# Kernel optimization log

Hardware: AMD Instinct MI355X
Metric: run time of the kernel (lower is better)

## Reference

```python
import jax, jax.numpy as jnp
import numpy as np

GENRES = 20; TAGS = 1000; GTAGS = 1128; MOVIES = 20000; YEARS = 120; TBINS = 128
B = 1024; HIST = 50; PH = 256; OD = 128
EG = 8; ET = 16; EGT = 16; EM = 32; EY = 8; EUG = 32; ETS = 4
PAD = MOVIES  # padding index; context buffers have MOVIES+1 rows, last row = zeros


def setup_inputs():
    ks = iter(jax.random.split(jax.random.key(0), 64))
    nrm = lambda shp, s=0.1: (s * jax.random.normal(next(ks), shp)).astype(jnp.float32)
    P = MOVIES + 1
    genome_ctx = jax.random.uniform(next(ks), (P, GTAGS), dtype=jnp.float32).at[-1].set(0.0)
    genre_ctx = jax.random.uniform(next(ks), (P, GENRES), dtype=jnp.float32).at[-1].set(0.0)
    tag_ctx = jax.random.uniform(next(ks), (P, TAGS), dtype=jnp.float32).at[-1].set(0.0)
    year_ctx = jax.random.randint(next(ks), (P,), 0, YEARS).at[-1].set(0)
    return dict(
        user_genre_contexts=jax.random.uniform(next(ks), (B, GENRES), dtype=jnp.float32),
        user_watch_history=jax.random.randint(next(ks), (B, HIST), 0, P),
        user_watch_history_ratings=5.0 * jax.random.uniform(next(ks), (B, HIST), dtype=jnp.float32),
        timestamps=jax.random.randint(next(ks), (B,), 0, TBINS),
        target_movieId=jax.random.randint(next(ks), (B,), 0, MOVIES),
        genome_ctx=genome_ctx, genre_ctx=genre_ctx, tag_ctx=tag_ctx, year_ctx=year_ctx,
        item_emb=nrm((P, EM), 0.01).at[-1].set(0.0),  # padding_idx row zeroed
        year_emb_tab=nrm((YEARS, EY), 0.01),
        ts_emb_tab=nrm((TBINS, ETS), 0.01),
        w_item=nrm((EM, EM)), b_item=jnp.zeros((EM,), jnp.float32),
        w_genre=nrm((GENRES, EG)), b_genre=jnp.zeros((EG,), jnp.float32),
        w_tag=nrm((TAGS, ET)), b_tag=jnp.zeros((ET,), jnp.float32),
        w_genome=nrm((GTAGS, EGT)), b_genome=jnp.zeros((EGT,), jnp.float32),
        w_year=nrm((EY, EY)), b_year=jnp.zeros((EY,), jnp.float32),
        w_ugenre=nrm((GENRES, EUG)), b_ugenre=jnp.zeros((EUG,), jnp.float32),
        w_ts=nrm((ETS, ETS)), b_ts=jnp.zeros((ETS,), jnp.float32),
        w_up1=nrm((OD + EGT + EUG + ETS, PH)), b_up1=jnp.zeros((PH,), jnp.float32),
        w_up2=nrm((PH, OD)), b_up2=jnp.zeros((OD,), jnp.float32),
        w_ip1=nrm((EG + ET + EGT + EM + EY, PH)), b_ip1=jnp.zeros((PH,), jnp.float32),
        w_ip2=nrm((PH, OD)), b_ip2=jnp.zeros((OD,), jnp.float32),
    )


def reference(user_genre_contexts, user_watch_history, user_watch_history_ratings,
              timestamps, target_movieId, genome_ctx, genre_ctx, tag_ctx, year_ctx,
              item_emb, year_emb_tab, ts_emb_tab,
              w_item, b_item, w_genre, b_genre, w_tag, b_tag, w_genome, b_genome,
              w_year, b_year, w_ugenre, b_ugenre, w_ts, b_ts,
              w_up1, b_up1, w_up2, b_up2, w_ip1, b_ip1, w_ip2, b_ip2):
    lt = lambda x, W, b: jnp.tanh(x @ W + b)

    def item_tower(mg, mt, mgt, yr, ids):
        # concat of five small Linear+Tanh towers, then 2-layer projection MLP
        cat = jnp.concatenate([
            lt(mg, w_genre, b_genre), lt(mt, w_tag, b_tag), lt(mgt, w_genome, b_genome),
            lt(item_emb[ids], w_item, b_item), lt(year_emb_tab[yr], w_year, b_year)], axis=-1)
        return jax.nn.relu(cat @ w_ip1 + b_ip1) @ w_ip2 + b_ip2

    Bn, Hn = user_watch_history.shape
    pad_mask = (user_watch_history != PAD).astype(jnp.float32)[..., None]       # (B,H,1)
    rating_weights = user_watch_history_ratings[..., None] * pad_mask            # (B,H,1)
    weight_sum = jnp.clip(jnp.abs(rating_weights).sum(axis=1), 1e-6)             # (B,1)

    # item pool: full item-tower embeddings of watched movies, rating-weighted avg
    flat = user_watch_history.reshape(-1)
    embs = item_tower(genre_ctx[flat], tag_ctx[flat], genome_ctx[flat],
                      year_ctx[flat], flat).reshape(Bn, Hn, OD)
    item_pool = (embs * rating_weights).sum(axis=1) / weight_sum                 # (B,OD)

    # genome pool (kept separately in use_item_pool_for_history mode)
    genome_embs = lt(genome_ctx[user_watch_history], w_genome, b_genome)         # (B,H,EGT)
    genome_emb = (genome_embs * rating_weights).sum(axis=1) / weight_sum

    genre_emb = lt(user_genre_contexts, w_ugenre, b_ugenre)
    ts_emb = lt(ts_emb_tab[timestamps], w_ts, b_ts)
    user_cat = jnp.concatenate([item_pool, genome_emb, genre_emb, ts_emb], axis=1)
    user = jax.nn.relu(user_cat @ w_up1 + b_up1) @ w_up2 + b_up2                 # (B,OD)

    item = item_tower(genre_ctx[target_movieId], tag_ctx[target_movieId],
                      genome_ctx[target_movieId], year_ctx[target_movieId], target_movieId)
    return jnp.einsum('bd,bd->b', user, item)
```

## Files before the change

### kernel.cpp

```cpp
#include <hip/hip_runtime.h>
#include <hip/hip_bf16.h>

typedef __bf16 bf16x8 __attribute__((ext_vector_type(8)));
typedef __bf16 bf16x4 __attribute__((ext_vector_type(4)));
typedef float  f32x4  __attribute__((ext_vector_type(4)));

namespace {
constexpr int P       = 20001;
constexpr int NT_TILE = 1251;
constexpr int PROWS   = NT_TILE * 16;
constexpr int NGENRES = 20;
constexpr int NTAGS   = 1000;
constexpr int NGTAGS  = 1128;
constexpr int NB      = 1024;
constexpr int NH      = 50;
constexpr int PHID    = 256;
constexpr int OD      = 128;
constexpr int EG = 8, ET = 16, EGT = 16, EM = 32, EY = 8, EUG = 32, ETS = 4;
constexpr int PAD  = 20000;
constexpr int SAW  = 1160;
constexpr int SC   = 104;
constexpr int SH   = 264;
constexpr int UC   = 192;
constexpr int UCS  = 200;
constexpr int KC_TAG = 32, KC_GEN = 36;
constexpr int KC_IP1 = 3,  NT_IP1 = 16;
constexpr int KC_IP2 = 8,  NT_IP2 = 8;
constexpr int KC_UP1 = 6,  NT_UP1 = 16;
constexpr int KC_UP2 = 8,  NT_UP2 = 8;
}

static __device__ __forceinline__ f32x4 mfma16(bf16x8 a, bf16x8 b, f32x4 c) {
  return __builtin_amdgcn_mfma_f32_16x16x32_bf16(a, b, c, 0, 0, 0);
}

__global__ __launch_bounds__(512) void setup_wf_kernel(
    const float* __restrict__ w_tag, const float* __restrict__ w_genome,
    const float* __restrict__ w_ip1, const float* __restrict__ w_ip2,
    const float* __restrict__ w_up1, const float* __restrict__ w_up2,
    __bf16* __restrict__ Wtf, __bf16* __restrict__ Wgf,
    __bf16* __restrict__ Wip1f, __bf16* __restrict__ Wip2f,
    __bf16* __restrict__ Wup1f, __bf16* __restrict__ Wup2f)
{
  const int b = blockIdx.x, t = threadIdx.x;
  const int l = t >> 3, j = t & 7;
  const int krow = (l >> 4) * 8 + j, l15 = l & 15;
  const float* src; __bf16* dst; int K, N, kc, nt;
  if (b < 32)        { src = w_tag;    dst = Wtf   + (long)b * 512;       K = NTAGS;  N = 16;  kc = b;      nt = 0; }
  else if (b < 68)   { int i = b - 32;  src = w_genome; dst = Wgf   + (long)i * 512; K = NGTAGS; N = 16;  kc = i;      nt = 0; }
  else if (b < 116)  { int i = b - 68;  src = w_ip1;    dst = Wip1f + (long)i * 512; K = 80;     N = 256; kc = i / 16; nt = i % 16; }
  else if (b < 180)  { int i = b - 116; src = w_ip2;    dst = Wip2f + (long)i * 512; K = 256;    N = 128; kc = i / 8;  nt = i % 8; }
  else if (b < 276)  { int i = b - 180; src = w_up1;    dst = Wup1f + (long)i * 512; K = 180;    N = 256; kc = i / 16; nt = i % 16; }
  else               { int i = b - 276; src = w_up2;    dst = Wup2f + (long)i * 512; K = 256;    N = 128; kc = i / 8;  nt = i % 8; }
  const int k = kc * 32 + krow, n = nt * 16 + l15;
  float v = (k < K) ? src[(long)k * N + n] : 0.f;
  dst[t] = (__bf16)v;
}

__global__ __launch_bounds__(256) void tower_kernel(
    const float* __restrict__ tag_ctx, const float* __restrict__ genome_ctx,
    const float* __restrict__ genre_ctx, const int* __restrict__ year_ctx,
    const float* __restrict__ item_emb, const float* __restrict__ year_tab,
    const float* __restrict__ w_genre, const float* __restrict__ b_genre,
    const float* __restrict__ b_tag,   const float* __restrict__ b_genome,
    const float* __restrict__ w_item,  const float* __restrict__ b_item,
    const float* __restrict__ w_year,  const float* __restrict__ b_year,
    const float* __restrict__ b_ip1,   const float* __restrict__ b_ip2,
    const __bf16* __restrict__ Wtf,   const __bf16* __restrict__ Wgf,
    const __bf16* __restrict__ Wip1f, const __bf16* __restrict__ Wip2f,
    float* __restrict__ T, float* __restrict__ GT)
{
  union ShU { __bf16 a[16][SAW]; __bf16 h[16][SH]; };
  __shared__ __align__(16) ShU u;
  __shared__ __align__(16) __bf16 s_cat[16][SC];
  __shared__ __align__(16) f32x4  s_red[3][64];

  const int t = threadIdx.x, tile = blockIdx.x;
  const int wave = t >> 6, lane = t & 63, l15 = lane & 15, quad = lane >> 4;
  const int r = t >> 4, c16 = t & 15;
  const long rid = min(tile * 16 + r, P - 1);

  {
    const float* row = tag_ctx + rid * NTAGS;
    #pragma unroll
    for (int i = 0; i < 16; ++i) {
      int f = c16 + i * 16;
      if (f < 250) {
        float4 v = *(const float4*)(row + f * 4);
        bf16x4 b4 = {(__bf16)v.x, (__bf16)v.y, (__bf16)v.z, (__bf16)v.w};
        *(bf16x4*)&u.a[r][f * 4] = b4;
      }
    }
    if (c16 < 8) *(bf16x4*)&u.a[r][NTAGS + c16 * 4] = (bf16x4){(__bf16)0.f,(__bf16)0.f,(__bf16)0.f,(__bf16)0.f};
  }
  __syncthreads();

  f32x4 accT = {0.f, 0.f, 0.f, 0.f};
  #pragma unroll
  for (int kc = 0; kc < 8; ++kc) {
    const int kcg = wave * 8 + kc;
    bf16x8 a  = *(const bf16x8*)&u.a[l15][kcg * 32 + quad * 8];
    bf16x8 bb = *(const bf16x8*)(Wtf + ((long)kcg * 64 + lane) * 8);
    accT = mfma16(a, bb, accT);
  }
  if (wave > 0) s_red[wave - 1][lane] = accT;
  __syncthreads();

  {
    const float* row = genome_ctx + rid * NGTAGS;
    #pragma unroll
    for (int i = 0; i < 18; ++i) {
      int f = c16 + i * 16;
      if (f < 282) {
        float4 v = *(const float4*)(row + f * 4);
        bf16x4 b4 = {(__bf16)v.x, (__bf16)v.y, (__bf16)v.z, (__bf16)v.w};
        *(bf16x4*)&u.a[r][f * 4] = b4;
      }
    }
    if (c16 < 8) *(bf16x4*)&u.a[r][NGTAGS + c16 * 4] = (bf16x4){(__bf16)0.f,(__bf16)0.f,(__bf16)0.f,(__bf16)0.f};
  }
  if (wave == 0) {
    accT += s_red[0][lane]; accT += s_red[1][lane]; accT += s_red[2][lane];
    const float bt = b_tag[l15];
    #pragma unroll
    for (int r2 = 0; r2 < 4; ++r2)
      s_cat[quad * 4 + r2][EG + l15] = (__bf16)tanhf(accT[r2] + bt);
  }
  __syncthreads();

  f32x4 accG = {0.f, 0.f, 0.f, 0.f};
  #pragma unroll
  for (int kc = 0; kc < 9; ++kc) {
    const int kcg = wave * 9 + kc;
    bf16x8 a  = *(const bf16x8*)&u.a[l15][kcg * 32 + quad * 8];
    bf16x8 bb = *(const bf16x8*)(Wgf + ((long)kcg * 64 + lane) * 8);
    accG = mfma16(a, bb, accG);
  }
  if (wave > 0) s_red[wave - 1][lane] = accG;
  __syncthreads();

  if (wave == 0) {
    accG += s_red[0][lane]; accG += s_red[1][lane]; accG += s_red[2][lane];
    const float bg = b_genome[l15];
    #pragma unroll
    for (int r2 = 0; r2 < 4; ++r2) {
      int m = quad * 4 + r2;
      float v = tanhf(accG[r2] + bg);
      s_cat[m][EG + ET + l15] = (__bf16)v;
      GT[(long)(tile * 16 + m) * EGT + l15] = v;
    }
  }
  {
    const int m = r, j = c16;
    const long id = rid;
    if (j < 8) {
      const float* rg = genre_ctx + id * NGENRES;
      float a = b_genre[j];
      #pragma unroll
      for (int k = 0; k < NGENRES; ++k) a = fmaf(rg[k], w_genre[k * EG + j], a);
      s_cat[m][j] = (__bf16)tanhf(a);
      s_cat[m][80 + j] = (__bf16)0.f;
      s_cat[m][88 + j] = (__bf16)0.f;
    } else {
      const int jj = j - 8;
      const int yr = year_ctx[id];
      float a = b_year[jj];
      #pragma unroll
      for (int k = 0; k < EY; ++k)
        a = fmaf(year_tab[yr * EY + k], w_year[k * EY + jj], a);
      s_cat[m][72 + jj] = (__bf16)tanhf(a);
    }
    const float* e = item_emb + id * EM;
    float a0 = b_item[2 * j], a1 = b_item[2 * j + 1];
    #pragma unroll 8
    for (int k = 0; k < EM; ++k) {
      float ev = e[k];
      a0 = fmaf(ev, w_item[k * EM + 2 * j], a0);
      a1 = fmaf(ev, w_item[k * EM + 2 * j + 1], a1);
    }
    s_cat[m][40 + 2 * j]     = (__bf16)tanhf(a0);
    s_cat[m][40 + 2 * j + 1] = (__bf16)tanhf(a1);
  }
  __syncthreads();

  {
    bf16x8 af[KC_IP1];
    #pragma unroll
    for (int kc = 0; kc < KC_IP1; ++kc)
      af[kc] = *(const bf16x8*)&s_cat[l15][kc * 32 + quad * 8];
    #pragma unroll
    for (int nt = 0; nt < 4; ++nt) {
      const int n = wave * 64 + nt * 16 + l15;
      const float bb = b_ip1[n];
      f32x4 acc = {bb, bb, bb, bb};
      #pragma unroll
      for (int kc = 0; kc < KC_IP1; ++kc) {
        bf16x8 bfr = *(const bf16x8*)(Wip1f + ((long)(kc * NT_IP1 + wave * 4 + nt) * 64 + lane) * 8);
        acc = mfma16(af[kc], bfr, acc);
      }
      #pragma unroll
      for (int r2 = 0; r2 < 4; ++r2)
        u.h[quad * 4 + r2][n] = (__bf16)fmaxf(acc[r2], 0.f);
    }
  }
  __syncthreads();

  {
    bf16x8 af[KC_IP2];
    #pragma unroll
    for (int kc = 0; kc < KC_IP2; ++kc)
      af[kc] = *(const bf16x8*)&u.h[l15][kc * 32 + quad * 8];
    #pragma unroll
    for (int nt = 0; nt < 2; ++nt) {
      const int n = wave * 32 + nt * 16 + l15;
      const float bb = b_ip2[n];
      f32x4 acc = {bb, bb, bb, bb};
      #pragma unroll
      for (int kc = 0; kc < KC_IP2; ++kc) {
        bf16x8 bfr = *(const bf16x8*)(Wip2f + ((long)(kc * NT_IP2 + wave * 2 + nt) * 64 + lane) * 8);
        acc = mfma16(af[kc], bfr, acc);
      }
      #pragma unroll
      for (int r2 = 0; r2 < 4; ++r2)
        T[(long)(tile * 16 + quad * 4 + r2) * OD + n] = acc[r2];
    }
  }
}

__global__ __launch_bounds__(256) void user_pool_kernel(
    const float* __restrict__ ugc, const int* __restrict__ hist,
    const float* __restrict__ ratings, const int* __restrict__ tstamps,
    const float* __restrict__ ts_tab,
    const float* __restrict__ w_ugenre, const float* __restrict__ b_ugenre,
    const float* __restrict__ w_ts, const float* __restrict__ b_ts,
    const float* __restrict__ T, const float* __restrict__ GT,
    __bf16* __restrict__ Ucat)
{
  __shared__ float s_w[64];
  __shared__ int   s_ids[64];
  __shared__ float s_part[2][OD];
  __shared__ float s_gp[8][EGT];
  __shared__ float s_inv;

  const int b = blockIdx.x, t = threadIdx.x;

  if (t < 64) {
    int id = PAD; float w = 0.f;
    if (t < NH) {
      id = hist[b * NH + t];
      float r = ratings[b * NH + t];
      w = (id != PAD) ? r : 0.f;
    }
    s_ids[t] = id; s_w[t] = w;
    float s = fabsf(w);
    #pragma unroll
    for (int off = 32; off; off >>= 1) s += __shfl_xor(s, off, 64);
    if (t == 0) s_inv = 1.f / fmaxf(s, 1e-6f);
  }
  __syncthreads();
  const float inv = s_inv;

  {
    const int c = t & (OD - 1), part = t >> 7;
    float acc = 0.f;
    #pragma unroll
    for (int i = 0; i < 25; ++i) {
      const int h = part * 25 + i;
      acc = fmaf(s_w[h], T[(long)s_ids[h] * OD + c], acc);
    }
    s_part[part][c] = acc;
  }
  __syncthreads();
  if (t < OD) {
    Ucat[(long)b * UC + t] = (__bf16)((s_part[0][t] + s_part[1][t]) * inv);
  } else {
    const int uu = t - 128, col = uu & 15, part = uu >> 4;
    float acc = 0.f;
    #pragma unroll
    for (int i = 0; i < 7; ++i) {
      const int h = part * 7 + i;
      if (h < NH) acc = fmaf(s_w[h], GT[(long)s_ids[h] * EGT + col], acc);
    }
    s_gp[part][col] = acc;
  }
  __syncthreads();
  if (t < EGT) {
    float acc = 0.f;
    #pragma unroll
    for (int p = 0; p < 8; ++p) acc += s_gp[p][t];
    Ucat[(long)b * UC + OD + t] = (__bf16)(acc * inv);
  } else if (t >= 32 && t < 64) {
    const int j = t - 32;
    float a = b_ugenre[j];
    #pragma unroll
    for (int k = 0; k < NGENRES; ++k)
      a = fmaf(ugc[b * NGENRES + k], w_ugenre[k * EUG + j], a);
    Ucat[(long)b * UC + 144 + j] = (__bf16)tanhf(a);
  } else if (t >= 64 && t < 64 + ETS) {
    const int j = t - 64;
    const int ts = tstamps[b];
    float a = b_ts[j];
    #pragma unroll
    for (int k = 0; k < ETS; ++k)
      a = fmaf(ts_tab[ts * ETS + k], w_ts[k * ETS + j], a);
    Ucat[(long)b * UC + 176 + j] = (__bf16)tanhf(a);
  } else if (t >= 68 && t < 80) {
    Ucat[(long)b * UC + 180 + (t - 68)] = (__bf16)0.f;
  }
}

__global__ __launch_bounds__(256) void user_mlp_kernel(
    const int* __restrict__ target,
    const float* __restrict__ b_up1, const float* __restrict__ b_up2,
    const __bf16* __restrict__ Wup1f, const __bf16* __restrict__ Wup2f,
    const __bf16* __restrict__ Ucat, const float* __restrict__ T,
    float* __restrict__ out)
{
  __shared__ __align__(16) __bf16 s_u[16][UCS];
  __shared__ __align__(16) __bf16 s_h[16][SH];
  __shared__ __align__(16) float  s_e[16][132];
  __shared__ float s_red[2];

  const int t = threadIdx.x, blk = blockIdx.x;
  const int wave = t >> 6, lane = t & 63, l15 = lane & 15, quad = lane >> 4;
  const int u0 = blk * 16;

  {
    const int uu = t >> 4, s = t & 15;
    const __bf16* src = Ucat + (long)(u0 + uu) * UC;
    *(bf16x8*)&s_u[uu][s * 8] = *(const bf16x8*)(src + s * 8);
    if (s < 8)
      *(bf16x8*)&s_u[uu][(s + 16) * 8] = *(const bf16x8*)(src + (s + 16) * 8);
  }
  __syncthreads();

  {
    bf16x8 af[KC_UP1];
    #pragma unroll
    for (int kc = 0; kc < KC_UP1; ++kc)
      af[kc] = *(const bf16x8*)&s_u[l15][kc * 32 + quad * 8];
    #pragma unroll
    for (int nt = 0; nt < 4; ++nt) {
      const int n = wave * 64 + nt * 16 + l15;
      const float bb = b_up1[n];
      f32x4 acc = {bb, bb, bb, bb};
      #pragma unroll
      for (int kc = 0; kc < KC_UP1; ++kc) {
        bf16x8 bfr = *(const bf16x8*)(Wup1f + ((long)(kc * NT_UP1 + wave * 4 + nt) * 64 + lane) * 8);
        acc = mfma16(af[kc], bfr, acc);
      }
      #pragma unroll
      for (int r2 = 0; r2 < 4; ++r2)
        s_h[quad * 4 + r2][n] = (__bf16)fmaxf(acc[r2], 0.f);
    }
  }
  __syncthreads();

  {
    bf16x8 af[KC_UP2];
    #pragma unroll
    for (int kc = 0; kc < KC_UP2; ++kc)
      af[kc] = *(const bf16x8*)&s_h[l15][kc * 32 + quad * 8];
    #pragma unroll
    for (int nt = 0; nt < 2; ++nt) {
      const int n = wave * 32 + nt * 16 + l15;
      const float bb = b_up2[n];
      f32x4 acc = {bb, bb, bb, bb};
      #pragma unroll
      for (int kc = 0; kc < KC_UP2; ++kc) {
        bf16x8 bfr = *(const bf16x8*)(Wup2f + ((long)(kc * NT_UP2 + wave * 2 + nt) * 64 + lane) * 8);
        acc = mfma16(af[kc], bfr, acc);
      }
      #pragma unroll
      for (int r2 = 0; r2 < 4; ++r2)
        s_e[quad * 4 + r2][n] = acc[r2];
    }
  }
  __syncthreads();

  if (t < 128) {
    const int uu = t >> 3, q = t & 7;
    const int tgt = target[u0 + uu];
    const float* trow = T + (long)tgt * OD + q * 16;
    float s = 0.f;
    #pragma unroll
    for (int i = 0; i < 4; ++i) {
      float4 v = *(const float4*)(trow + i * 4);
      f32x4 e = *(const f32x4*)&s_e[uu][q * 16 + i * 4];
      s += v.x * e[0] + v.y * e[1] + v.z * e[2] + v.w * e[3];
    }
    s += __shfl_down(s, 1, 64);
    s += __shfl_down(s, 2, 64);
    s += __shfl_down(s, 4, 64);
    if (q == 0) out[u0 + uu] = s;
  }
  (void)s_red;
}

extern "C" void kernel_launch(void* const* d_in, const int* in_sizes, int n_in,
                              void* d_out, int out_size, void* d_ws, size_t ws_size,
                              hipStream_t stream) {
  const float* ugc      = (const float*)d_in[0];
  const int*   hist     = (const int*)  d_in[1];
  const float* ratings  = (const float*)d_in[2];
  const int*   tstamps  = (const int*)  d_in[3];
  const int*   target   = (const int*)  d_in[4];
  const float* genome   = (const float*)d_in[5];
  const float* genrec   = (const float*)d_in[6];
  const float* tagc     = (const float*)d_in[7];
  const int*   yearc    = (const int*)  d_in[8];
  const float* item_emb = (const float*)d_in[9];
  const float* year_tab = (const float*)d_in[10];
  const float* ts_tab   = (const float*)d_in[11];
  const float* w_item   = (const float*)d_in[12];
  const float* b_item   = (const float*)d_in[13];
  const float* w_genre  = (const float*)d_in[14];
  const float* b_genre  = (const float*)d_in[15];
  const float* w_tag    = (const float*)d_in[16];
  const float* b_tag    = (const float*)d_in[17];
  const float* w_genome = (const float*)d_in[18];
  const float* b_genome = (const float*)d_in[19];
  const float* w_year   = (const float*)d_in[20];
  const float* b_year   = (const float*)d_in[21];
  const float* w_ugenre = (const float*)d_in[22];
  const float* b_ugenre = (const float*)d_in[23];
  const float* w_ts     = (const float*)d_in[24];
  const float* b_ts     = (const float*)d_in[25];
  const float* w_up1    = (const float*)d_in[26];
  const float* b_up1    = (const float*)d_in[27];
  const float* w_up2    = (const float*)d_in[28];
  const float* b_up2    = (const float*)d_in[29];
  const float* w_ip1    = (const float*)d_in[30];
  const float* b_ip1    = (const float*)d_in[31];
  const float* w_ip2    = (const float*)d_in[32];
  const float* b_ip2    = (const float*)d_in[33];

  char* ws = (char*)d_ws;
  size_t off = 0;
  float*  T     = (float*) (ws + off); off += (size_t)PROWS * OD * 4;
  float*  GT    = (float*) (ws + off); off += (size_t)PROWS * EGT * 4;
  __bf16* Ucat  = (__bf16*)(ws + off); off += (size_t)NB * UC * 2;
  __bf16* Wtf   = (__bf16*)(ws + off); off += (size_t)KC_TAG * 512 * 2;
  __bf16* Wgf   = (__bf16*)(ws + off); off += (size_t)KC_GEN * 512 * 2;
  __bf16* Wip1f = (__bf16*)(ws + off); off += (size_t)KC_IP1 * NT_IP1 * 512 * 2;
  __bf16* Wip2f = (__bf16*)(ws + off); off += (size_t)KC_IP2 * NT_IP2 * 512 * 2;
  __bf16* Wup1f = (__bf16*)(ws + off); off += (size_t)KC_UP1 * NT_UP1 * 512 * 2;
  __bf16* Wup2f = (__bf16*)(ws + off); off += (size_t)KC_UP2 * NT_UP2 * 512 * 2;

  setup_wf_kernel<<<dim3(340), dim3(512), 0, stream>>>(
      w_tag, w_genome, w_ip1, w_ip2, w_up1, w_up2,
      Wtf, Wgf, Wip1f, Wip2f, Wup1f, Wup2f);

  tower_kernel<<<dim3(NT_TILE), dim3(256), 0, stream>>>(
      tagc, genome, genrec, yearc, item_emb, year_tab,
      w_genre, b_genre, b_tag, b_genome, w_item, b_item, w_year, b_year,
      b_ip1, b_ip2, Wtf, Wgf, Wip1f, Wip2f, T, GT);

  user_pool_kernel<<<dim3(NB), dim3(256), 0, stream>>>(
      ugc, hist, ratings, tstamps, ts_tab,
      w_ugenre, b_ugenre, w_ts, b_ts, T, GT, Ucat);

  user_mlp_kernel<<<dim3(NB / 16), dim3(256), 0, stream>>>(
      target, b_up1, b_up2, Wup1f, Wup2f, Ucat, T, (float*)d_out);
}
```

Baseline: 284.7 us.

## Load tag/genome rows straight into MFMA A-fragments, dropping LDS staging

The tower kernel no longer stages whole tag and genome context rows through a large shared-memory buffer. Each lane now reads its 8-element slice from global memory, converts it to bf16 in registers and feeds the MFMA directly. Separate reduction buffers let the tag and genome reductions be finished by different waves after one shared barrier. The goal is to cut LDS footprint and barriers so more blocks fit per CU (launch bounds now ask for 4). The cost is scattered 32-byte per-lane global loads instead of coalesced row loads.

```diff
diff --git a/kernel.cpp b/kernel.cpp
--- a/kernel.cpp
+++ b/kernel.cpp
@@ -18,7 +18,6 @@
 constexpr int OD      = 128;
 constexpr int EG = 8, ET = 16, EGT = 16, EM = 32, EY = 8, EUG = 32, ETS = 4;
 constexpr int PAD  = 20000;
-constexpr int SAW  = 1160;
 constexpr int SC   = 104;
 constexpr int SH   = 264;
 constexpr int UC   = 192;
@@ -57,7 +56,7 @@
   dst[t] = (__bf16)v;
 }
 
-__global__ __launch_bounds__(256) void tower_kernel(
+__global__ __launch_bounds__(256, 4) void tower_kernel(
     const float* __restrict__ tag_ctx, const float* __restrict__ genome_ctx,
     const float* __restrict__ genre_ctx, const int* __restrict__ year_ctx,
     const float* __restrict__ item_emb, const float* __restrict__ year_tab,
@@ -70,89 +69,66 @@
     const __bf16* __restrict__ Wip1f, const __bf16* __restrict__ Wip2f,
     float* __restrict__ T, float* __restrict__ GT)
 {
-  union ShU { __bf16 a[16][SAW]; __bf16 h[16][SH]; };
-  __shared__ __align__(16) ShU u;
   __shared__ __align__(16) __bf16 s_cat[16][SC];
-  __shared__ __align__(16) f32x4  s_red[3][64];
+  __shared__ __align__(16) __bf16 s_h[16][SH];
+  __shared__ __align__(16) f32x4  s_redT[3][64];
+  __shared__ __align__(16) f32x4  s_redG[3][64];
 
   const int t = threadIdx.x, tile = blockIdx.x;
   const int wave = t >> 6, lane = t & 63, l15 = lane & 15, quad = lane >> 4;
   const int r = t >> 4, c16 = t & 15;
-  const long rid = min(tile * 16 + r, P - 1);
-
-  {
-    const float* row = tag_ctx + rid * NTAGS;
-    #pragma unroll
-    for (int i = 0; i < 16; ++i) {
-      int f = c16 + i * 16;
-      if (f < 250) {
-        float4 v = *(const float4*)(row + f * 4);
-        bf16x4 b4 = {(__bf16)v.x, (__bf16)v.y, (__bf16)v.z, (__bf16)v.w};
-        *(bf16x4*)&u.a[r][f * 4] = b4;
-      }
-    }
-    if (c16 < 8) *(bf16x4*)&u.a[r][NTAGS + c16 * 4] = (bf16x4){(__bf16)0.f,(__bf16)0.f,(__bf16)0.f,(__bf16)0.f};
-  }
-  __syncthreads();
+  const long rid   = min(tile * 16 + l15, P - 1);
+  const long rid_r = min(tile * 16 + r,   P - 1);
 
   f32x4 accT = {0.f, 0.f, 0.f, 0.f};
-  #pragma unroll
-  for (int kc = 0; kc < 8; ++kc) {
-    const int kcg = wave * 8 + kc;
-    bf16x8 a  = *(const bf16x8*)&u.a[l15][kcg * 32 + quad * 8];
-    bf16x8 bb = *(const bf16x8*)(Wtf + ((long)kcg * 64 + lane) * 8);
-    accT = mfma16(a, bb, accT);
-  }
-  if (wave > 0) s_red[wave - 1][lane] = accT;
-  __syncthreads();
-
-  {
-    const float* row = genome_ctx + rid * NGTAGS;
-    #pragma unroll
-    for (int i = 0; i < 18; ++i) {
-      int f = c16 + i * 16;
-      if (f < 282) {
-        float4 v = *(const float4*)(row + f * 4);
-        bf16x4 b4 = {(__bf16)v.x, (__bf16)v.y, (__bf16)v.z, (__bf16)v.w};
-        *(bf16x4*)&u.a[r][f * 4] = b4;
-      }
-    }
-    if (c16 < 8) *(bf16x4*)&u.a[r][NGTAGS + c16 * 4] = (bf16x4){(__bf16)0.f,(__bf16)0.f,(__bf16)0.f,(__bf16)0.f};
-  }
-  if (wave == 0) {
-    accT += s_red[0][lane]; accT += s_red[1][lane]; accT += s_red[2][lane];
-    const float bt = b_tag[l15];
-    #pragma unroll
-    for (int r2 = 0; r2 < 4; ++r2)
-      s_cat[quad * 4 + r2][EG + l15] = (__bf16)tanhf(accT[r2] + bt);
-  }
-  __syncthreads();
+  {
+    const float* trow = tag_ctx + rid * NTAGS;
+    #pragma unroll
+    for (int kc = 0; kc < 8; ++kc) {
+      const int kcg = wave * 8 + kc;
+      const int col = kcg * 32 + quad * 8;
+      bf16x8 a;
+      if (col < NTAGS) {
+        const float4 v0 = *(const float4*)(trow + col);
+        const float4 v1 = *(const float4*)(trow + col + 4);
+        a = (bf16x8){(__bf16)v0.x, (__bf16)v0.y, (__bf16)v0.z, (__bf16)v0.w,
+                     (__bf16)v1.x, (__bf16)v1.y, (__bf16)v1.z, (__bf16)v1.w};
+      } else {
+        a = (bf16x8){(__bf16)0.f,(__bf16)0.f,(__bf16)0.f,(__bf16)0.f,
+                     (__bf16)0.f,(__bf16)0.f,(__bf16)0.f,(__bf16)0.f};
+      }
+      bf16x8 bb = *(const bf16x8*)(Wtf + ((long)kcg * 64 + lane) * 8);
+      accT = mfma16(a, bb, accT);
+    }
+  }
+  if (wave > 0) s_redT[wave - 1][lane] = accT;
 
   f32x4 accG = {0.f, 0.f, 0.f, 0.f};
-  #pragma unroll
-  for (int kc = 0; kc < 9; ++kc) {
-    const int kcg = wave * 9 + kc;
-    bf16x8 a  = *(const bf16x8*)&u.a[l15][kcg * 32 + quad * 8];
-    bf16x8 bb = *(const bf16x8*)(Wgf + ((long)kcg * 64 + lane) * 8);
-    accG = mfma16(a, bb, accG);
-  }
-  if (wave > 0) s_red[wave - 1][lane] = accG;
-  __syncthreads();
-
-  if (wave == 0) {
-    accG += s_red[0][lane]; accG += s_red[1][lane]; accG += s_red[2][lane];
-    const float bg = b_genome[l15];
-    #pragma unroll
-    for (int r2 = 0; r2 < 4; ++r2) {
-      int m = quad * 4 + r2;
-      float v = tanhf(accG[r2] + bg);
-      s_cat[m][EG + ET + l15] = (__bf16)v;
-      GT[(long)(tile * 16 + m) * EGT + l15] = v;
-    }
-  }
+  {
+    const float* grow = genome_ctx + rid * NGTAGS;
+    #pragma unroll
+    for (int kc = 0; kc < 9; ++kc) {
+      const int kcg = wave * 9 + kc;
+      const int col = kcg * 32 + quad * 8;
+      bf16x8 a;
+      if (col < NGTAGS) {
+        const float4 v0 = *(const float4*)(grow + col);
+        const float4 v1 = *(const float4*)(grow + col + 4);
+        a = (bf16x8){(__bf16)v0.x, (__bf16)v0.y, (__bf16)v0.z, (__bf16)v0.w,
+                     (__bf16)v1.x, (__bf16)v1.y, (__bf16)v1.z, (__bf16)v1.w};
+      } else {
+        a = (bf16x8){(__bf16)0.f,(__bf16)0.f,(__bf16)0.f,(__bf16)0.f,
+                     (__bf16)0.f,(__bf16)0.f,(__bf16)0.f,(__bf16)0.f};
+      }
+      bf16x8 bb = *(const bf16x8*)(Wgf + ((long)kcg * 64 + lane) * 8);
+      accG = mfma16(a, bb, accG);
+    }
+  }
+  if (wave != 1) s_redG[wave ? wave - 1 : 0][lane] = accG;
+
   {
     const int m = r, j = c16;
-    const long id = rid;
+    const long id = rid_r;
     if (j < 8) {
       const float* rg = genre_ctx + id * NGENRES;
       float a = b_genre[j];
@@ -183,6 +159,25 @@
   }
   __syncthreads();
 
+  if (wave == 0) {
+    accT += s_redT[0][lane]; accT += s_redT[1][lane]; accT += s_redT[2][lane];
+    const float bt = b_tag[l15];
+    #pragma unroll
+    for (int r2 = 0; r2 < 4; ++r2)
+      s_cat[quad * 4 + r2][EG + l15] = (__bf16)tanhf(accT[r2] + bt);
+  } else if (wave == 1) {
+    accG += s_redG[0][lane]; accG += s_redG[1][lane]; accG += s_redG[2][lane];
+    const float bg = b_genome[l15];
+    #pragma unroll
+    for (int r2 = 0; r2 < 4; ++r2) {
+      int m = quad * 4 + r2;
+      float v = tanhf(accG[r2] + bg);
+      s_cat[m][EG + ET + l15] = (__bf16)v;
+      GT[(long)(tile * 16 + m) * EGT + l15] = v;
+    }
+  }
+  __syncthreads();
+
   {
     bf16x8 af[KC_IP1];
     #pragma unroll
@@ -200,7 +195,7 @@
       }
       #pragma unroll
       for (int r2 = 0; r2 < 4; ++r2)
-        u.h[quad * 4 + r2][n] = (__bf16)fmaxf(acc[r2], 0.f);
+        s_h[quad * 4 + r2][n] = (__bf16)fmaxf(acc[r2], 0.f);
     }
   }
   __syncthreads();
@@ -209,7 +204,7 @@
     bf16x8 af[KC_IP2];
     #pragma unroll
     for (int kc = 0; kc < KC_IP2; ++kc)
-      af[kc] = *(const bf16x8*)&u.h[l15][kc * 32 + quad * 8];
+      af[kc] = *(const bf16x8*)&s_h[l15][kc * 32 + quad * 8];
     #pragma unroll
     for (int nt = 0; nt < 2; ++nt) {
       const int n = wave * 32 + nt * 16 + l15;
```

Result: no change. 290.2 us (+1.9%).
